# Optimization experiments

Hardware: AMD Instinct MI355X
Metric: run time of the kernel (lower is better)

Reference implementation:

```python
import jax, jax.numpy as jnp
import numpy as np


def setup_inputs() -> dict:
    key = jax.random.key(0)
    k1, k2 = jax.random.split(key)
    # x: [B, C_meg, T, c_in] -- NHWC where H is the MEG sensor axis (split axis 1 in original)
    x = jax.random.normal(k1, (8, 160, 1024, 1), dtype=jnp.float32)
    # W: [kh=1, kw=7, c_in=1, filters=32] conv kernel (self.conv.weights[0]; bias is never applied)
    W = jax.random.normal(k2, (1, 7, 1, 32), dtype=jnp.float32) * 0.1
    return {"x": x, "W": W}


def reference(x, W):
    # Original: for each sensor pair (i, j != i), conv2d(x_i + x_j, W), then max over j,
    # stacked over i -> [B, C, T, F].
    # Conv is linear and bias-free, so conv(x_i + x_j) = y_i + y_j where y = conv(x).
    # Hence out_i = y_i + max_{j != i} y_j  (exact algebraic rewrite, O(C) convs not O(C^2)).
    y = jax.lax.conv_general_dilated(
        x, W, window_strides=(1, 1), padding="SAME",
        dimension_numbers=("NHWC", "HWIO", "NHWC"),
    )  # [B, C, T, F] (kh=1 => per-sensor-row temporal conv, same as original per-slice conv)

    yt = jnp.moveaxis(y, 1, -1)               # [B, T, F, C]
    vals, idx = jax.lax.top_k(yt, 2)          # top-2 over sensor axis
    m1 = vals[..., 0:1]                       # global max over channels
    m2 = vals[..., 1:2]                       # second max
    am = idx[..., 0:1]                        # argmax channel
    C = yt.shape[-1]
    # max over j != i: equals m1 unless i is the argmax, then m2
    max_other = jnp.where(am == jnp.arange(C), m2, m1)  # [B, T, F, C]
    out = yt + max_other
    return jnp.moveaxis(out, -1, 1)           # [B, C, T, F]
```

## Files before the change

kernel.cpp:

```cpp
#include <hip/hip_runtime.h>


#define WT 16
#define BLOCK 256

__global__ __launch_bounds__(BLOCK)
void pcc_kernel(const float* __restrict__ x,
                const float* __restrict__ Wf,
                float* __restrict__ out) {
    __shared__ float xs[160][WT + 6];

    const int n  = blockIdx.x >> 6;
    const int wt = blockIdx.x & 63;
    const int w0 = wt * WT;
    const int tid = threadIdx.x;

    const float* xn = x + (size_t)n * 160 * 1024;
    for (int idx = tid; idx < 160 * (WT + 6); idx += BLOCK) {
        int row = idx / (WT + 6);
        int col = idx - row * (WT + 6);
        int gw  = w0 - 3 + col;
        float v = 0.f;
        if (gw >= 0 && gw < 1024) v = xn[row * 1024 + gw];
        xs[row][col] = v;
    }
    __syncthreads();

    const int cpair = tid & 15;
    const int c0    = cpair * 2;
    const int wl    = tid >> 4;

    float wg0[7], wg1[7];
#pragma unroll
    for (int k = 0; k < 7; ++k) {
        wg0[k] = Wf[k * 32 + c0];
        wg1[k] = Wf[k * 32 + c0 + 1];
    }

    float m1a = -INFINITY, m2a = -INFINITY;
    float m1b = -INFINITY, m2b = -INFINITY;
    int ama = 0, amb = 0;

    for (int h = 0; h < 160; ++h) {
        float xw[7];
#pragma unroll
        for (int j = 0; j < 7; ++j) xw[j] = xs[h][wl + j];
        float ya = 0.f, yb = 0.f;
#pragma unroll
        for (int j = 0; j < 7; ++j) {
            ya = fmaf(xw[j], wg0[j], ya);
            yb = fmaf(xw[j], wg1[j], yb);
        }
        bool ga = ya > m1a;
        m2a = ga ? m1a : fmaxf(m2a, ya);
        m1a = ga ? ya  : m1a;
        ama = ga ? h   : ama;
        bool gb = yb > m1b;
        m2b = gb ? m1b : fmaxf(m2b, yb);
        m1b = gb ? yb  : m1b;
        amb = gb ? h   : amb;
    }

    float* obase = out + ((size_t)(n * 160) * 1024 + (w0 + wl)) * 32 + c0;
    for (int h = 0; h < 160; ++h) {
        float xw[7];
#pragma unroll
        for (int j = 0; j < 7; ++j) xw[j] = xs[h][wl + j];
        float ya = 0.f, yb = 0.f;
#pragma unroll
        for (int j = 0; j < 7; ++j) {
            ya = fmaf(xw[j], wg0[j], ya);
            yb = fmaf(xw[j], wg1[j], yb);
        }
        float oa = ya + (h == ama ? m2a : m1a);
        float ob = yb + (h == amb ? m2b : m1b);
        float2 v; v.x = oa; v.y = ob;
        *reinterpret_cast<float2*>(obase + (size_t)h * 1024 * 32) = v;
    }
}

extern "C" void kernel_launch(void* const* d_in, const int* in_sizes, int n_in,
                              void* d_out, int out_size, void* d_ws, size_t ws_size,
                              hipStream_t stream) {
    const float* x  = (const float*)d_in[0];
    const float* Wf = (const float*)d_in[1];
    float* out = (float*)d_out;
    dim3 grid(8 * (1024 / WT));
    dim3 block(BLOCK);
    pcc_kernel<<<grid, block, 0, stream>>>(x, Wf, out);
}
```

Measured before the change: 186.3 us.

## Map one thread per output channel and halve time tile to double block count

Changes each thread from computing two adjacent channels (float2 stores) to computing a single channel, with 32 threads covering the channels for each time position, and halves the time tile from 16 to 8, doubling the grid. The intent is more parallelism and blocks per device, with fully coalesced 128-byte scalar stores per wavefront row, and fewer registers per thread. In exchange, shared-memory reads of x are no longer amortised across two channels, the halo overhead per tile grows, and stores shrink from 8 to 4 bytes per thread.

```diff
diff --git a/kernel.cpp b/kernel.cpp
--- a/kernel.cpp
+++ b/kernel.cpp
@@ -1,7 +1,7 @@
 #include <hip/hip_runtime.h>
 
 
-#define WT 16
+#define WT 8
 #define BLOCK 256
 
 __global__ __launch_bounds__(BLOCK)
@@ -10,8 +10,8 @@
                 float* __restrict__ out) {
     __shared__ float xs[160][WT + 6];
 
-    const int n  = blockIdx.x >> 6;
-    const int wt = blockIdx.x & 63;
+    const int n  = blockIdx.x >> 7;
+    const int wt = blockIdx.x & 127;
     const int w0 = wt * WT;
     const int tid = threadIdx.x;
 
@@ -26,56 +26,34 @@
     }
     __syncthreads();
 
-    const int cpair = tid & 15;
-    const int c0    = cpair * 2;
-    const int wl    = tid >> 4;
+    const int c  = tid & 31;
+    const int wl = tid >> 5;
 
-    float wg0[7], wg1[7];
+    float wg[7];
 #pragma unroll
-    for (int k = 0; k < 7; ++k) {
-        wg0[k] = Wf[k * 32 + c0];
-        wg1[k] = Wf[k * 32 + c0 + 1];
+    for (int k = 0; k < 7; ++k) wg[k] = Wf[k * 32 + c];
+
+    float m1 = -INFINITY, m2 = -INFINITY;
+    int am = 0;
+
+#pragma unroll 4
+    for (int h = 0; h < 160; ++h) {
+        float y = 0.f;
+#pragma unroll
+        for (int j = 0; j < 7; ++j) y = fmaf(xs[h][wl + j], wg[j], y);
+        bool g = y > m1;
+        m2 = g ? m1 : fmaxf(m2, y);
+        m1 = g ? y  : m1;
+        am = g ? h  : am;
     }
 
-    float m1a = -INFINITY, m2a = -INFINITY;
-    float m1b = -INFINITY, m2b = -INFINITY;
-    int ama = 0, amb = 0;
-
+    float* obase = out + ((size_t)(n * 160) * 1024 + (w0 + wl)) * 32 + c;
+#pragma unroll 4
     for (int h = 0; h < 160; ++h) {
-        float xw[7];
+        float y = 0.f;
 #pragma unroll
-        for (int j = 0; j < 7; ++j) xw[j] = xs[h][wl + j];
-        float ya = 0.f, yb = 0.f;
-#pragma unroll
-        for (int j = 0; j < 7; ++j) {
-            ya = fmaf(xw[j], wg0[j], ya);
-            yb = fmaf(xw[j], wg1[j], yb);
-        }
-        bool ga = ya > m1a;
-        m2a = ga ? m1a : fmaxf(m2a, ya);
-        m1a = ga ? ya  : m1a;
-        ama = ga ? h   : ama;
-        bool gb = yb > m1b;
-        m2b = gb ? m1b : fmaxf(m2b, yb);
-        m1b = gb ? yb  : m1b;
-        amb = gb ? h   : amb;
-    }
-
-    float* obase = out + ((size_t)(n * 160) * 1024 + (w0 + wl)) * 32 + c0;
-    for (int h = 0; h < 160; ++h) {
-        float xw[7];
-#pragma unroll
-        for (int j = 0; j < 7; ++j) xw[j] = xs[h][wl + j];
-        float ya = 0.f, yb = 0.f;
-#pragma unroll
-        for (int j = 0; j < 7; ++j) {
-            ya = fmaf(xw[j], wg0[j], ya);
-            yb = fmaf(xw[j], wg1[j], yb);
-        }
-        float oa = ya + (h == ama ? m2a : m1a);
-        float ob = yb + (h == amb ? m2b : m1b);
-        float2 v; v.x = oa; v.y = ob;
-        *reinterpret_cast<float2*>(obase + (size_t)h * 1024 * 32) = v;
+        for (int j = 0; j < 7; ++j) y = fmaf(xs[h][wl + j], wg[j], y);
+        obase[(size_t)h * 1024 * 32] = y + (h == am ? m2 : m1);
     }
 }
 
```

After: 185.2 us. Within noise of the previous version (-0.6%).

## Remap threads to one channel and two time steps with float2 LDS reads

Applied to the files above, without the earlier changes.

Each thread now owns one filter channel and two adjacent time positions instead of two channels at one time position. This lets it load its input window as four aligned float2 LDS reads, shares the window across both outputs, and needs only seven weight registers. The LDS row is padded to 24 floats for alignment. The inner loops get explicit unroll pragmas. Output stores become two scalar stores per row instead of one float2, which changes the write coalescing pattern; across the wavefront the stores still cover contiguous 128-byte channel runs.

```diff
diff --git a/kernel.cpp b/kernel.cpp
--- a/kernel.cpp
+++ b/kernel.cpp
@@ -1,14 +1,15 @@
 #include <hip/hip_runtime.h>
 
 
-#define WT 16
 #define BLOCK 256
+#define WT    16
+#define LDSW  24
 
 __global__ __launch_bounds__(BLOCK)
 void pcc_kernel(const float* __restrict__ x,
                 const float* __restrict__ Wf,
                 float* __restrict__ out) {
-    __shared__ float xs[160][WT + 6];
+    __shared__ __align__(16) float xs[160][LDSW];
 
     const int n  = blockIdx.x >> 6;
     const int wt = blockIdx.x & 63;
@@ -16,9 +17,9 @@
     const int tid = threadIdx.x;
 
     const float* xn = x + (size_t)n * 160 * 1024;
-    for (int idx = tid; idx < 160 * (WT + 6); idx += BLOCK) {
-        int row = idx / (WT + 6);
-        int col = idx - row * (WT + 6);
+    for (int idx = tid; idx < 160 * LDSW; idx += BLOCK) {
+        int row = idx / LDSW;
+        int col = idx - row * LDSW;
         int gw  = w0 - 3 + col;
         float v = 0.f;
         if (gw >= 0 && gw < 1024) v = xn[row * 1024 + gw];
@@ -26,31 +27,32 @@
     }
     __syncthreads();
 
-    const int cpair = tid & 15;
-    const int c0    = cpair * 2;
-    const int wl    = tid >> 4;
+    const int c = tid & 31;
+    const int t = tid >> 5;
 
-    float wg0[7], wg1[7];
+    float wg[7];
 #pragma unroll
-    for (int k = 0; k < 7; ++k) {
-        wg0[k] = Wf[k * 32 + c0];
-        wg1[k] = Wf[k * 32 + c0 + 1];
-    }
+    for (int k = 0; k < 7; ++k) wg[k] = Wf[k * 32 + c];
+
 
     float m1a = -INFINITY, m2a = -INFINITY;
     float m1b = -INFINITY, m2b = -INFINITY;
     int ama = 0, amb = 0;
 
+#pragma unroll 4
     for (int h = 0; h < 160; ++h) {
-        float xw[7];
-#pragma unroll
-        for (int j = 0; j < 7; ++j) xw[j] = xs[h][wl + j];
+        const float2* row = reinterpret_cast<const float2*>(&xs[h][2 * t]);
+        float2 d0 = row[0], d1 = row[1], d2 = row[2], d3 = row[3];
+        float f0 = d0.x, f1 = d0.y, f2 = d1.x, f3 = d1.y;
+        float f4 = d2.x, f5 = d2.y, f6 = d3.x, f7 = d3.y;
         float ya = 0.f, yb = 0.f;
-#pragma unroll
-        for (int j = 0; j < 7; ++j) {
-            ya = fmaf(xw[j], wg0[j], ya);
-            yb = fmaf(xw[j], wg1[j], yb);
-        }
+        ya = fmaf(f0, wg[0], ya); yb = fmaf(f1, wg[0], yb);
+        ya = fmaf(f1, wg[1], ya); yb = fmaf(f2, wg[1], yb);
+        ya = fmaf(f2, wg[2], ya); yb = fmaf(f3, wg[2], yb);
+        ya = fmaf(f3, wg[3], ya); yb = fmaf(f4, wg[3], yb);
+        ya = fmaf(f4, wg[4], ya); yb = fmaf(f5, wg[4], yb);
+        ya = fmaf(f5, wg[5], ya); yb = fmaf(f6, wg[5], yb);
+        ya = fmaf(f6, wg[6], ya); yb = fmaf(f7, wg[6], yb);
         bool ga = ya > m1a;
         m2a = ga ? m1a : fmaxf(m2a, ya);
         m1a = ga ? ya  : m1a;
@@ -61,21 +63,24 @@
         amb = gb ? h   : amb;
     }
 
-    float* obase = out + ((size_t)(n * 160) * 1024 + (w0 + wl)) * 32 + c0;
+    float* obase = out + ((size_t)(n * 160) * 1024 + (w0 + 2 * t)) * 32 + c;
+#pragma unroll 2
     for (int h = 0; h < 160; ++h) {
-        float xw[7];
-#pragma unroll
-        for (int j = 0; j < 7; ++j) xw[j] = xs[h][wl + j];
+        const float2* row = reinterpret_cast<const float2*>(&xs[h][2 * t]);
+        float2 d0 = row[0], d1 = row[1], d2 = row[2], d3 = row[3];
+        float f0 = d0.x, f1 = d0.y, f2 = d1.x, f3 = d1.y;
+        float f4 = d2.x, f5 = d2.y, f6 = d3.x, f7 = d3.y;
         float ya = 0.f, yb = 0.f;
-#pragma unroll
-        for (int j = 0; j < 7; ++j) {
-            ya = fmaf(xw[j], wg0[j], ya);
-            yb = fmaf(xw[j], wg1[j], yb);
-        }
-        float oa = ya + (h == ama ? m2a : m1a);
-        float ob = yb + (h == amb ? m2b : m1b);
-        float2 v; v.x = oa; v.y = ob;
-        *reinterpret_cast<float2*>(obase + (size_t)h * 1024 * 32) = v;
+        ya = fmaf(f0, wg[0], ya); yb = fmaf(f1, wg[0], yb);
+        ya = fmaf(f1, wg[1], ya); yb = fmaf(f2, wg[1], yb);
+        ya = fmaf(f2, wg[2], ya); yb = fmaf(f3, wg[2], yb);
+        ya = fmaf(f3, wg[3], ya); yb = fmaf(f4, wg[3], yb);
+        ya = fmaf(f4, wg[4], ya); yb = fmaf(f5, wg[4], yb);
+        ya = fmaf(f5, wg[5], ya); yb = fmaf(f6, wg[5], yb);
+        ya = fmaf(f6, wg[6], ya); yb = fmaf(f7, wg[6], yb);
+        float* orow = obase + (size_t)h * 1024 * 32;
+        orow[0]  = ya + (h == ama ? m2a : m1a);
+        orow[32] = yb + (h == amb ? m2b : m1b);
     }
 }
 
```

Measured after the change: 192.3 us. +3.2%, slower.
